# Performance work log

Measured on AMD Instinct MI355X. Metric: run time of the kernel, lower is better.

## Reference

```python
import jax, jax.numpy as jnp
import numpy as np

B, C, H, N, M = 4, 256, 4, 2048, 2048
D = C // H  # head_dim
BN_EPS = 1e-5


def conv1x1(W, b, x):
    # nn.Conv1d(Cin, Cout, kernel_size=1): x [B, Cin, N] -> [B, Cout, N]
    return jnp.einsum('oc,bcn->bon', W, x) + b[None, :, None]


def setup_inputs() -> dict:
    key = jax.random.key(0)
    ks = jax.random.split(key, 10)
    w = lambda k, shape: (jax.random.normal(k, shape, jnp.float32) * 0.05)
    return {
        'x1': jax.random.normal(ks[0], (B, C, N), jnp.float32),
        'x2': jax.random.normal(ks[1], (B, C, M), jnp.float32),
        'kv_mask': jax.random.randint(ks[2], (B, M), 0, 2).astype(bool),
        'Wq': w(ks[3], (C, C)), 'bq': jnp.zeros((C,), jnp.float32),
        'Wk': w(ks[4], (C, C)), 'bk': jnp.zeros((C,), jnp.float32),
        'Wv': w(ks[5], (C, C)), 'bv': jnp.zeros((C,), jnp.float32),
        'Wmh': w(ks[6], (C, C)), 'bmh': jnp.zeros((C,), jnp.float32),
        'W1': w(ks[7], (2 * C, 2 * C)), 'b1': jnp.zeros((2 * C,), jnp.float32),
        'bn_gamma': jnp.ones((2 * C,), jnp.float32),
        'bn_beta': jnp.zeros((2 * C,), jnp.float32),
        'bn_mean': jnp.zeros((2 * C,), jnp.float32),
        'bn_var': jnp.ones((2 * C,), jnp.float32),
        'W2': w(ks[8], (C, 2 * C)), 'b2': jnp.zeros((C,), jnp.float32),
    }


def reference(x1, x2, kv_mask, Wq, bq, Wk, bk, Wv, bv, Wmh, bmh,
              W1, b1, bn_gamma, bn_beta, bn_mean, bn_var, W2, b2):
    bsz = x1.shape[0]
    # 1x1-conv Q/K/V projections, reshaped to [B, H, D, N]
    q = conv1x1(Wq, bq, x1).reshape(bsz, H, D, -1)
    k = conv1x1(Wk, bk, x2).reshape(bsz, H, D, -1)
    v = conv1x1(Wv, bv, x2).reshape(bsz, H, D, -1)

    # full attention: scores [B, H, N, M]
    QK = jnp.einsum('bhdn,bhdm->bhnm', q, k)
    # masked_fill happens BEFORE the 1/sqrt(D) scaling in the original
    QK = jnp.where(kv_mask[:, None, None, :], QK, jnp.float32(-1e6))
    score = jax.nn.softmax(QK / np.float32(np.sqrt(D)), axis=-1)
    add_value = jnp.einsum('bhnm,bhdm->bhdn', score, v).reshape(bsz, H * D, -1)

    add_value = conv1x1(Wmh, bmh, add_value)

    # cat_filter: conv1x1 -> BatchNorm1d (inference stats) -> ReLU -> conv1x1
    cat = jnp.concatenate([x1, add_value], axis=1)  # [B, 2C, N]
    h = conv1x1(W1, b1, cat)
    h = (h - bn_mean[None, :, None]) / jnp.sqrt(bn_var[None, :, None] + BN_EPS)
    h = bn_gamma[None, :, None] * h + bn_beta[None, :, None]
    h = jax.nn.relu(h)
    return x1 + conv1x1(W2, b2, h)
```

## Files before the change

kernel.cpp:

```cpp
#include <hip/hip_runtime.h>
#include <hip/hip_bf16.h>

#define SEQN 2048
#define SEQM 2048
#define CDIM 256
#define NB   4
#define NH   4
#define RDYMAGIC 0x7A3F19C5u

using bf16x8 = __attribute__((ext_vector_type(8))) short;
using f32x4  = __attribute__((ext_vector_type(4))) float;

__device__ inline unsigned short f2bf(float x) {
    __hip_bfloat16 h = __float2bfloat16(x);
    return *reinterpret_cast<unsigned short*>(&h);
}

__global__ __launch_bounds__(256, 4) void qkv_k(
    const float* __restrict__ Wq, const float* __restrict__ Wk,
    const float* __restrict__ Wv,
    const float* __restrict__ x1, const float* __restrict__ x2,
    const float* __restrict__ bq, const float* __restrict__ bk,
    const float* __restrict__ bv,
    unsigned short* __restrict__ qbf, unsigned short* __restrict__ kbf,
    unsigned short* __restrict__ vbf,
    const int* __restrict__ kvm, int* __restrict__ pidx, int* __restrict__ mcnt,
    unsigned int* __restrict__ rdy, float qscale)
{
    __shared__ __align__(16) char qsm[35840];
    const int bid = blockIdx.x, tid = threadIdx.x;

    if (bid < NB) {
        int* sc = reinterpret_cast<int*>(qsm);
        const int b = bid;
        int loc[8], c = 0;
        #pragma unroll
        for (int e = 0; e < 8; ++e) {
            loc[e] = (kvm[(size_t)b * SEQM + tid * 8 + e] != 0) ? 1 : 0;
            c += loc[e];
        }
        sc[tid] = c;
        __syncthreads();
        for (int off = 1; off < 256; off <<= 1) {
            int v = (tid >= off) ? sc[tid - off] : 0;
            __syncthreads();
            sc[tid] += v;
            __syncthreads();
        }
        int p = sc[tid] - c;
        if (tid == 255) mcnt[b] = sc[255];
        #pragma unroll
        for (int e = 0; e < 8; ++e) {
            pidx[(size_t)b * SEQM + tid * 8 + e] = loc[e] ? p : -1;
            p += loc[e];
        }
        __threadfence();
        __syncthreads();
        if (tid == 0)
            __hip_atomic_store(&rdy[b], RDYMAGIC, __ATOMIC_RELEASE,
                               __HIP_MEMORY_SCOPE_AGENT);
        return;
    }

    const int g = bid - NB;
    const int z = g >> 8, t = g & 255;
    const int bx = t & 1, by = t >> 1;

    short (*At)[72] = reinterpret_cast<short(*)[72]>(qsm);
    float (*Ts)[68] = reinterpret_cast<float(*)[68]>(qsm + 18432);

    const float* W = (z == 0) ? Wq : (z == 1) ? Wk : Wv;
    const float* X = (z == 0) ? x1 : x2;
    const float* bias = (z == 0) ? bq : (z == 1) ? bk : bv;

    const int w = tid >> 6, l = tid & 63, lm = l & 15, lg = l >> 4;
    const int o0 = bx * 128, ng0 = by * 64;
    const int b = ng0 >> 11, n0 = ng0 & 2047;
    const int wo = (w >> 1) * 64, wn = (w & 1) * 32;

    f32x4 acc[4][2] = {};
    const int arow = tid >> 2, acol = (tid & 3) * 16;
    const int tr = tid >> 2, tc = (tid & 3) * 16;
    const int tg = (((tc >> 4) ^ ((tr >> 3) & 3)) << 4);

    for (int k0 = 0; k0 < 256; k0 += 64) {
        __syncthreads();
        #pragma unroll
        for (int p = 0; p < 2; ++p) {
            const float* s = &W[(size_t)(o0 + arow + 64 * p) * 256 + k0 + acol];
            unsigned int u[8];
            #pragma unroll
            for (int q = 0; q < 4; ++q) {
                float4 f = *reinterpret_cast<const float4*>(&s[4 * q]);
                u[2 * q]     = (unsigned int)f2bf(f.x) | ((unsigned int)f2bf(f.y) << 16);
                u[2 * q + 1] = (unsigned int)f2bf(f.z) | ((unsigned int)f2bf(f.w) << 16);
            }
            *reinterpret_cast<uint4*>(&At[arow + 64 * p][acol]) =
                make_uint4(u[0], u[1], u[2], u[3]);
            *reinterpret_cast<uint4*>(&At[arow + 64 * p][acol + 8]) =
                make_uint4(u[4], u[5], u[6], u[7]);
        }
        {
            const float* s = &X[((size_t)b * CDIM + k0 + tr) * SEQN + n0 + tc];
            #pragma unroll
            for (int q = 0; q < 4; ++q)
                *reinterpret_cast<float4*>(&Ts[tr][tg + 4 * q]) =
                    *reinterpret_cast<const float4*>(&s[4 * q]);
        }
        __syncthreads();
        #pragma unroll
        for (int kc = 0; kc < 2; ++kc) {
            bf16x8 a[4], bf[2];
            #pragma unroll
            for (int i = 0; i < 4; ++i)
                a[i] = *reinterpret_cast<const bf16x8*>(&At[wo + 16 * i + lm][kc * 32 + lg * 8]);
            #pragma unroll
            for (int j = 0; j < 2; ++j) {
                const int bk0 = kc * 32 + lg * 8;
                const int gcol = (((((wn >> 4) + j)) ^ ((bk0 >> 3) & 3)) << 4) | lm;
                union { unsigned int u[4]; bf16x8 v; } cv;
                #pragma unroll
                for (int e = 0; e < 4; ++e) {
                    float lo = Ts[bk0 + 2 * e][gcol];
                    float hi = Ts[bk0 + 2 * e + 1][gcol];
                    cv.u[e] = (unsigned int)f2bf(lo) | ((unsigned int)f2bf(hi) << 16);
                }
                bf[j] = cv.v;
            }
            #pragma unroll
            for (int i = 0; i < 4; ++i)
                #pragma unroll
                for (int j = 0; j < 2; ++j)
                    acc[i][j] = __builtin_amdgcn_mfma_f32_16x16x32_bf16(a[i], bf[j], acc[i][j], 0, 0, 0);
        }
    }

    if (z != 0) {
        if (tid == 0) {
            while (__hip_atomic_load(&rdy[b], __ATOMIC_ACQUIRE,
                                     __HIP_MEMORY_SCOPE_AGENT) != RDYMAGIC)
                __builtin_amdgcn_s_sleep(2);
        }
        __syncthreads();
    }

    #pragma unroll
    for (int j = 0; j < 2; ++j) {
        const int ng = ng0 + wn + 16 * j + lm;
        const int bb = ng >> 11, n = ng & 2047;
        const int pos = (z == 0) ? n : pidx[(size_t)bb * SEQM + n];
        #pragma unroll
        for (int i = 0; i < 4; ++i) {
            const int ob = o0 + wo + 16 * i + 4 * lg;
            float4 bv4 = *reinterpret_cast<const float4*>(&bias[ob]);
            float v[4] = {acc[i][j][0] + bv4.x, acc[i][j][1] + bv4.y,
                          acc[i][j][2] + bv4.z, acc[i][j][3] + bv4.w};
            if (z == 2) {
                if (pos >= 0) {
                    #pragma unroll
                    for (int r = 0; r < 4; ++r)
                        vbf[((size_t)bb * CDIM + ob + r) * SEQM + pos] = f2bf(v[r]);
                }
            } else if (pos >= 0) {
                const int hh = ob >> 6, dbase = ob & 63;
                const float sc_ = (z == 0) ? qscale : 1.0f;
                ushort4 pk;
                pk.x = f2bf(v[0] * sc_); pk.y = f2bf(v[1] * sc_);
                pk.z = f2bf(v[2] * sc_); pk.w = f2bf(v[3] * sc_);
                unsigned short* dst = (z == 0) ? qbf : kbf;
                *reinterpret_cast<ushort4*>(
                    &dst[(((size_t)bb * NH + hh) * SEQN + pos) * 64 + dbase]) = pk;
            }
        }
    }
}

__device__ void do_attn(char* smraw,
    const unsigned short* __restrict__ qbf, const unsigned short* __restrict__ kbf,
    const unsigned short* __restrict__ vbf, const int* __restrict__ mcntg,
    unsigned short* __restrict__ catT, int bx, int h, int b)
{
    short (*Ks)[64][64] = reinterpret_cast<short(*)[64][64]>(smraw);
    short (*Vs)[64][64] = reinterpret_cast<short(*)[64][64]>(smraw + 16384);
    unsigned int (*Ps)[16][36] = reinterpret_cast<unsigned int(*)[16][36]>(smraw + 32768);

    const int tid = threadIdx.x;
    const int w = tid >> 6, l = tid & 63;
    const int lm = l & 15, lg = l >> 4;
    const int n_base = bx * 64 + w * 16;
    const size_t bhN = (size_t)(b * NH + h) * SEQN;
    const size_t cBase = (size_t)b * CDIM + h * 64;

    const int mcnt = mcntg[b];
    const int ntiles = (mcnt + 63) >> 6;

    if (ntiles == 0) {
        #pragma unroll
        for (int r = 0; r < 4; ++r) {
            int n = n_base + 4 * lg + r;
            unsigned short* dst = &catT[((size_t)b * SEQN + n) * 512 + 256 + h * 64];
            #pragma unroll
            for (int t = 0; t < 4; ++t) dst[16 * t + lm] = 0;
        }
        return;
    }

    const size_t qrow = (bhN + n_base + lm) * 64;
    bf16x8 qa0 = *reinterpret_cast<const bf16x8*>(&qbf[qrow + lg * 8]);
    bf16x8 qa1 = *reinterpret_cast<const bf16x8*>(&qbf[qrow + 32 + lg * 8]);

    f32x4 oacc[4] = {};
    float mrun = -3.0e5f, lrun = 0.f;

    const int r0 = tid >> 3, c8 = (tid & 7) * 8;
    const int c8s = c8 ^ ((r0 & 7) << 3);
    const int colr0 = (lg * 8) ^ ((lm & 7) << 3);
    const int colr1 = (32 + lg * 8) ^ ((lm & 7) << 3);

    {
        bf16x8 kr[2], vr[2];
        #pragma unroll
        for (int p = 0; p < 2; ++p) {
            kr[p] = *reinterpret_cast<const bf16x8*>(&kbf[(bhN + r0 + 32 * p) * 64 + c8]);
            vr[p] = *reinterpret_cast<const bf16x8*>(&vbf[(cBase + r0 + 32 * p) * SEQM + c8]);
        }
        #pragma unroll
        for (int p = 0; p < 2; ++p) {
            *reinterpret_cast<bf16x8*>(&Ks[0][r0 + 32 * p][c8s]) = kr[p];
            *reinterpret_cast<bf16x8*>(&Vs[0][r0 + 32 * p][c8s]) = vr[p];
        }
    }
    __syncthreads();

    for (int t64 = 0; t64 < ntiles; ++t64) {
        const int cur = t64 & 1;
        const bool has_next = (t64 < ntiles - 1);
        const int m0n = (t64 + 1) * 64;

        bf16x8 kr[2], vr[2];
        if (has_next) {
            #pragma unroll
            for (int p = 0; p < 2; ++p) {
                kr[p] = *reinterpret_cast<const bf16x8*>(
                    &kbf[(bhN + m0n + r0 + 32 * p) * 64 + c8]);
                vr[p] = *reinterpret_cast<const bf16x8*>(
                    &vbf[(cBase + r0 + 32 * p) * SEQM + m0n + c8]);
            }
        }

        f32x4 sv[4];
        __builtin_amdgcn_s_setprio(1);
        #pragma unroll
        for (int t = 0; t < 4; ++t) {
            bf16x8 ka0 = *reinterpret_cast<const bf16x8*>(&Ks[cur][16 * t + lm][colr0]);
            bf16x8 ka1 = *reinterpret_cast<const bf16x8*>(&Ks[cur][16 * t + lm][colr1]);
            f32x4 z = {0.f, 0.f, 0.f, 0.f};
            z = __builtin_amdgcn_mfma_f32_16x16x32_bf16(ka0, qa0, z, 0, 0, 0);
            z = __builtin_amdgcn_mfma_f32_16x16x32_bf16(ka1, qa1, z, 0, 0, 0);
            sv[t] = z;
        }
        __builtin_amdgcn_s_setprio(0);

        float mx = fmaxf(fmaxf(fmaxf(sv[0][0], sv[0][1]), fmaxf(sv[0][2], sv[0][3])),
                         fmaxf(fmaxf(sv[1][0], sv[1][1]), fmaxf(sv[1][2], sv[1][3])));
        mx = fmaxf(mx, fmaxf(fmaxf(fmaxf(sv[2][0], sv[2][1]), fmaxf(sv[2][2], sv[2][3])),
                             fmaxf(fmaxf(sv[3][0], sv[3][1]), fmaxf(sv[3][2], sv[3][3]))));
        mx = fmaxf(mx, __shfl_xor(mx, 16));
        mx = fmaxf(mx, __shfl_xor(mx, 32));
        const bool grew = (mx > mrun);
        float mnew = fmaxf(mrun, mx);
        float scl = exp2f(mrun - mnew);
        mrun = mnew;

        float rsum = 0.f;
        const int mrem = mcnt - t64 * 64;
        if (mrem >= 64) {
            #pragma unroll
            for (int t = 0; t < 4; ++t) {
                float p0 = exp2f(sv[t][0] - mnew);
                float p1 = exp2f(sv[t][1] - mnew);
                float p2 = exp2f(sv[t][2] - mnew);
                float p3 = exp2f(sv[t][3] - mnew);
                rsum += (p0 + p1) + (p2 + p3);
                unsigned int u0 = __builtin_amdgcn_perm(
                    __float_as_uint(p1), __float_as_uint(p0), 0x07060302u);
                unsigned int u1 = __builtin_amdgcn_perm(
                    __float_as_uint(p3), __float_as_uint(p2), 0x07060302u);
                *reinterpret_cast<uint2*>(&Ps[w][lm][8 * t + 2 * lg]) = make_uint2(u0, u1);
            }
        } else {
            #pragma unroll
            for (int t = 0; t < 4; ++t) {
                const int mb = 16 * t + 4 * lg;
                float p0 = (mb + 0 < mrem) ? exp2f(sv[t][0] - mnew) : 0.f;
                float p1 = (mb + 1 < mrem) ? exp2f(sv[t][1] - mnew) : 0.f;
                float p2 = (mb + 2 < mrem) ? exp2f(sv[t][2] - mnew) : 0.f;
                float p3 = (mb + 3 < mrem) ? exp2f(sv[t][3] - mnew) : 0.f;
                rsum += (p0 + p1) + (p2 + p3);
                unsigned int u0 = __builtin_amdgcn_perm(
                    __float_as_uint(p1), __float_as_uint(p0), 0x07060302u);
                unsigned int u1 = __builtin_amdgcn_perm(
                    __float_as_uint(p3), __float_as_uint(p2), 0x07060302u);
                *reinterpret_cast<uint2*>(&Ps[w][lm][8 * t + 2 * lg]) = make_uint2(u0, u1);
            }
        }
        rsum += __shfl_xor(rsum, 16);
        rsum += __shfl_xor(rsum, 32);
        lrun = lrun * scl + rsum;

        if (__any(grew && scl < 1.f)) {
            float sr[4];
            #pragma unroll
            for (int r = 0; r < 4; ++r) sr[r] = __shfl(scl, 4 * lg + r);
            #pragma unroll
            for (int t = 0; t < 4; ++t)
                #pragma unroll
                for (int r = 0; r < 4; ++r)
                    oacc[t][r] *= sr[r];
        }

        bf16x8 pa0 = *reinterpret_cast<const bf16x8*>(&Ps[w][lm][4 * lg]);
        bf16x8 pa1 = *reinterpret_cast<const bf16x8*>(&Ps[w][lm][16 + 4 * lg]);
        __builtin_amdgcn_s_setprio(1);
        #pragma unroll
        for (int t = 0; t < 4; ++t) {
            bf16x8 vb0 = *reinterpret_cast<const bf16x8*>(&Vs[cur][16 * t + lm][colr0]);
            bf16x8 vb1 = *reinterpret_cast<const bf16x8*>(&Vs[cur][16 * t + lm][colr1]);
            oacc[t] = __builtin_amdgcn_mfma_f32_16x16x32_bf16(pa0, vb0, oacc[t], 0, 0, 0);
            oacc[t] = __builtin_amdgcn_mfma_f32_16x16x32_bf16(pa1, vb1, oacc[t], 0, 0, 0);
        }
        __builtin_amdgcn_s_setprio(0);

        if (has_next) {
            const int nxt = cur ^ 1;
            #pragma unroll
            for (int p = 0; p < 2; ++p) {
                *reinterpret_cast<bf16x8*>(&Ks[nxt][r0 + 32 * p][c8s]) = kr[p];
                *reinterpret_cast<bf16x8*>(&Vs[nxt][r0 + 32 * p][c8s]) = vr[p];
            }
        }
        __syncthreads();
    }

    #pragma unroll
    for (int r = 0; r < 4; ++r) {
        float rinv = 1.f / __shfl(lrun, 4 * lg + r);
        int n = n_base + 4 * lg + r;
        unsigned short* dst = &catT[((size_t)b * SEQN + n) * 512 + 256 + h * 64];
        #pragma unroll
        for (int t = 0; t < 4; ++t)
            dst[16 * t + lm] = f2bf(oacc[t][r] * rinv);
    }
}

__global__ __launch_bounds__(256) void fused2_k(
    const unsigned short* __restrict__ qbf, const unsigned short* __restrict__ kbf,
    const unsigned short* __restrict__ vbf, const int* __restrict__ mcnt,
    unsigned short* __restrict__ catT,
    const float* __restrict__ W1, const float* __restrict__ b1,
    const float* __restrict__ gamma, const float* __restrict__ beta,
    const float* __restrict__ mean, const float* __restrict__ var,
    const float* __restrict__ Wmh, const float* __restrict__ bmh,
    unsigned short* __restrict__ Acat, float* __restrict__ cvec,
    const float* __restrict__ x1,
    const float* __restrict__ W2, unsigned short* __restrict__ W2b)
{
    __shared__ __align__(16) char smraw[41984];
    const int bid = blockIdx.x, tid = threadIdx.x;

    if (bid < 512) {
        do_attn(smraw, qbf, kbf, vbf, mcnt, catT,
                bid & 31, (bid >> 5) & 3, bid >> 7);
    } else if (bid < 1024) {
        const int j = bid - 512;
        const int c = tid;
        const float s = gamma[j] * rsqrtf(var[j] + 1e-5f);
        const float* w1b = W1 + (size_t)j * 512 + 256;
        Acat[(size_t)j * 512 + c] = f2bf(s * W1[(size_t)j * 512 + c]);
        float acc = 0.f;
        for (int t = 0; t < 256; ++t)
            acc += w1b[t] * Wmh[(size_t)t * 256 + c];
        Acat[(size_t)j * 512 + 256 + c] = f2bf(s * acc);
        if (c == 0) {
            float ab = 0.f;
            for (int t = 0; t < 256; ++t) ab += w1b[t] * bmh[t];
            cvec[j] = s * (b1[j] + ab - mean[j]) + beta[j];
        }
    } else if (bid < 1536) {
        const int t = bid - 1024;
        float (*Ts)[68] = reinterpret_cast<float(*)[68]>(smraw);
        const int cx = t & 3, ny = (t >> 2) & 31, b = t >> 7;
        const int c0 = cx * 64, n0 = ny * 64;
        const int cr = tid >> 2, nc = (tid & 3) * 16;
        #pragma unroll
        for (int q = 0; q < 4; ++q) {
            float4 v = *reinterpret_cast<const float4*>(
                &x1[((size_t)b * CDIM + c0 + cr) * SEQN + n0 + nc + 4 * q]);
            *reinterpret_cast<float4*>(&Ts[cr][nc + 4 * q]) = v;
        }
        __syncthreads();
        const int nr = tid >> 2, cc = (tid & 3) * 16;
        unsigned short tmp[16];
        #pragma unroll
        for (int e = 0; e < 16; ++e) tmp[e] = f2bf(Ts[cc + e][nr]);
        unsigned short* dp = &catT[((size_t)(b * SEQN + n0 + nr)) * 512 + c0 + cc];
        #pragma unroll
        for (int q = 0; q < 4; ++q)
            *reinterpret_cast<ushort4*>(&dp[4 * q]) = *reinterpret_cast<ushort4*>(&tmp[4 * q]);
    } else {
        const int cid = bid - 1536;
        const int idx = (cid * 256 + tid) * 4;
        float4 v = *reinterpret_cast<const float4*>(&W2[idx]);
        ushort4 p; p.x = f2bf(v.x); p.y = f2bf(v.y); p.z = f2bf(v.z); p.w = f2bf(v.w);
        *reinterpret_cast<ushort4*>(&W2b[idx]) = p;
    }
}

template<int OMODE>
__global__ __launch_bounds__(256) void gemm_mfma_k(
    const unsigned short* __restrict__ W, const unsigned short* __restrict__ X,
    const float* __restrict__ bias, const float* __restrict__ res,
    unsigned short* __restrict__ obf, float* __restrict__ ofp,
    int K, int ldx)
{
    __shared__ short At[128][72];
    __shared__ short Bt[64][72];
    const int tid = threadIdx.x;
    const int w = tid >> 6, l = tid & 63, lm = l & 15, lg = l >> 4;
    const int o0 = blockIdx.x * 128, ng0 = blockIdx.y * 64;
    const int wo = (w >> 1) * 64, wn = (w & 1) * 32;

    f32x4 acc[4][2] = {};
    const int arow = tid >> 2, acol = (tid & 3) * 16;

    for (int k0 = 0; k0 < K; k0 += 64) {
        __syncthreads();
        #pragma unroll
        for (int p = 0; p < 2; ++p) {
            const unsigned short* s = &W[(size_t)(o0 + arow + 64 * p) * K + k0 + acol];
            *reinterpret_cast<bf16x8*>(&At[arow + 64 * p][acol]) =
                *reinterpret_cast<const bf16x8*>(s);
            *reinterpret_cast<bf16x8*>(&At[arow + 64 * p][acol + 8]) =
                *reinterpret_cast<const bf16x8*>(s + 8);
        }
        {
            const unsigned short* s = &X[(size_t)(ng0 + arow) * ldx + k0 + acol];
            *reinterpret_cast<bf16x8*>(&Bt[arow][acol]) =
                *reinterpret_cast<const bf16x8*>(s);
            *reinterpret_cast<bf16x8*>(&Bt[arow][acol + 8]) =
                *reinterpret_cast<const bf16x8*>(s + 8);
        }
        __syncthreads();
        #pragma unroll
        for (int kc = 0; kc < 2; ++kc) {
            bf16x8 a[4], bf[2];
            #pragma unroll
            for (int i = 0; i < 4; ++i)
                a[i] = *reinterpret_cast<const bf16x8*>(&At[wo + 16 * i + lm][kc * 32 + lg * 8]);
            #pragma unroll
            for (int j = 0; j < 2; ++j)
                bf[j] = *reinterpret_cast<const bf16x8*>(&Bt[wn + 16 * j + lm][kc * 32 + lg * 8]);
            #pragma unroll
            for (int i = 0; i < 4; ++i)
                #pragma unroll
                for (int j = 0; j < 2; ++j)
                    acc[i][j] = __builtin_amdgcn_mfma_f32_16x16x32_bf16(a[i], bf[j], acc[i][j], 0, 0, 0);
        }
    }

    #pragma unroll
    for (int j = 0; j < 2; ++j) {
        const int ng = ng0 + wn + 16 * j + lm;
        const int b = ng >> 11, n = ng & 2047;
        #pragma unroll
        for (int i = 0; i < 4; ++i) {
            const int ob = o0 + wo + 16 * i + 4 * lg;
            float4 bv = *reinterpret_cast<const float4*>(&bias[ob]);
            float v[4] = {acc[i][j][0] + bv.x, acc[i][j][1] + bv.y,
                          acc[i][j][2] + bv.z, acc[i][j][3] + bv.w};
            if (OMODE == 2) {
                ushort4 pk;
                pk.x = f2bf(fmaxf(v[0], 0.f)); pk.y = f2bf(fmaxf(v[1], 0.f));
                pk.z = f2bf(fmaxf(v[2], 0.f)); pk.w = f2bf(fmaxf(v[3], 0.f));
                *reinterpret_cast<ushort4*>(&obf[(size_t)ng * 512 + ob]) = pk;
            } else {
                #pragma unroll
                for (int r = 0; r < 4; ++r) {
                    size_t ad = ((size_t)b * CDIM + ob + r) * SEQN + n;
                    ofp[ad] = v[r] + res[ad];
                }
            }
        }
    }
}

extern "C" void kernel_launch(void* const* d_in, const int* in_sizes, int n_in,
                              void* d_out, int out_size, void* d_ws, size_t ws_size,
                              hipStream_t stream)
{
    (void)in_sizes; (void)n_in; (void)out_size; (void)ws_size;
    const float* x1    = (const float*)d_in[0];
    const float* x2    = (const float*)d_in[1];
    const int*   kvm   = (const int*)  d_in[2];
    const float* Wq    = (const float*)d_in[3];
    const float* bq    = (const float*)d_in[4];
    const float* Wk    = (const float*)d_in[5];
    const float* bk    = (const float*)d_in[6];
    const float* Wv    = (const float*)d_in[7];
    const float* bv    = (const float*)d_in[8];
    const float* Wmh   = (const float*)d_in[9];
    const float* bmh   = (const float*)d_in[10];
    const float* W1    = (const float*)d_in[11];
    const float* b1    = (const float*)d_in[12];
    const float* gamma = (const float*)d_in[13];
    const float* beta  = (const float*)d_in[14];
    const float* mean  = (const float*)d_in[15];
    const float* var   = (const float*)d_in[16];
    const float* W2    = (const float*)d_in[17];
    const float* b2    = (const float*)d_in[18];
    float* out = (float*)d_out;

    const size_t act = (size_t)NB * CDIM * SEQN;
    unsigned short* ws    = (unsigned short*)d_ws;
    unsigned short* qbf   = ws;
    unsigned short* kbf   = qbf   + act;
    unsigned short* vbf   = kbf   + act;
    unsigned short* catT  = vbf   + act;
    unsigned short* hbuf  = catT  + 2 * act;
    unsigned short* W2b   = hbuf  + 2 * act;
    unsigned short* Acat  = W2b   + 131072;
    float*          cvec  = (float*)(Acat + 262144);
    int*            pidx  = (int*)(cvec + 512);
    int*            mcnt  = pidx + (size_t)NB * SEQM;
    unsigned int*   rdy   = (unsigned int*)(mcnt + 16);

    const float qscale = 0.125f * 1.44269504088896f;

    qkv_k<<<dim3(NB + 768), dim3(256), 0, stream>>>(
        Wq, Wk, Wv, x1, x2, bq, bk, bv, qbf, kbf, vbf,
        kvm, pidx, mcnt, rdy, qscale);

    fused2_k<<<dim3(1664), dim3(256), 0, stream>>>(
        qbf, kbf, vbf, mcnt, catT,
        W1, b1, gamma, beta, mean, var, Wmh, bmh, Acat, cvec,
        x1, W2, W2b);

    gemm_mfma_k<2><<<dim3(4, 128), dim3(256), 0, stream>>>(
        Acat, catT, cvec, nullptr, hbuf, nullptr, 512, 512);

    gemm_mfma_k<3><<<dim3(2, 128), dim3(256), 0, stream>>>(
        W2b, hbuf, b2, x1, nullptr, out, 512, 512);
}
```

Measured before the change: 78.12 us.

## Fuse the two final GEMMs into one launch with per-tile counter handoff

Merges the W1 (BN+ReLU) GEMM and the W2 residual GEMM into a single kernel. Consumer blocks spin on a per-column-tile atomic counter until all four producer row-blocks have written that hbuf tile, which removes one launch and lets the two stages overlap. The block-index mappings in the QKV and attention kernels are also reordered to group tiles per XCD for cache locality. The risks are spin-wait deadlock if consumers occupy CUs before producers run (ordering by block id mitigates this) and the extra counter reset.

```diff
diff --git a/kernel.cpp b/kernel.cpp
--- a/kernel.cpp
+++ b/kernel.cpp
@@ -25,12 +25,14 @@
     unsigned short* __restrict__ qbf, unsigned short* __restrict__ kbf,
     unsigned short* __restrict__ vbf,
     const int* __restrict__ kvm, int* __restrict__ pidx, int* __restrict__ mcnt,
-    unsigned int* __restrict__ rdy, float qscale)
+    unsigned int* __restrict__ rdy, unsigned int* __restrict__ hcnt,
+    float qscale)
 {
     __shared__ __align__(16) char qsm[35840];
     const int bid = blockIdx.x, tid = threadIdx.x;
 
     if (bid < NB) {
+        if (bid == 0 && tid < 128) hcnt[tid] = 0;
         int* sc = reinterpret_cast<int*>(qsm);
         const int b = bid;
         int loc[8], c = 0;
@@ -64,7 +66,7 @@
 
     const int g = bid - NB;
     const int z = g >> 8, t = g & 255;
-    const int bx = t & 1, by = t >> 1;
+    const int bx = t >> 7, by = t & 127;
 
     short (*At)[72] = reinterpret_cast<short(*)[72]>(qsm);
     float (*Ts)[68] = reinterpret_cast<float(*)[68]>(qsm + 18432);
@@ -369,8 +371,10 @@
     const int bid = blockIdx.x, tid = threadIdx.x;
 
     if (bid < 512) {
-        do_attn(smraw, qbf, kbf, vbf, mcnt, catT,
-                bid & 31, (bid >> 5) & 3, bid >> 7);
+        const int xcd = bid & 7, slot = bid >> 3;
+        const int p = xcd * 2 + (slot >> 5);
+        const int qt = slot & 31;
+        do_attn(smraw, qbf, kbf, vbf, mcnt, catT, qt, p & 3, p >> 2);
     } else if (bid < 1024) {
         const int j = bid - 512;
         const int c = tid;
@@ -416,35 +420,54 @@
     }
 }
 
-template<int OMODE>
-__global__ __launch_bounds__(256) void gemm_mfma_k(
-    const unsigned short* __restrict__ W, const unsigned short* __restrict__ X,
-    const float* __restrict__ bias, const float* __restrict__ res,
-    unsigned short* __restrict__ obf, float* __restrict__ ofp,
-    int K, int ldx)
+__global__ __launch_bounds__(256) void gemm23_k(
+    const unsigned short* __restrict__ Acat, const float* __restrict__ cvec,
+    const unsigned short* __restrict__ W2b, const float* __restrict__ b2,
+    const float* __restrict__ x1,
+    const unsigned short* __restrict__ catT, unsigned short* __restrict__ hbuf,
+    float* __restrict__ out, unsigned int* __restrict__ hcnt)
 {
     __shared__ short At[128][72];
     __shared__ short Bt[64][72];
-    const int tid = threadIdx.x;
+    const int bid = blockIdx.x, tid = threadIdx.x;
     const int w = tid >> 6, l = tid & 63, lm = l & 15, lg = l >> 4;
-    const int o0 = blockIdx.x * 128, ng0 = blockIdx.y * 64;
+    const int arow = tid >> 2, acol = (tid & 3) * 16;
     const int wo = (w >> 1) * 64, wn = (w & 1) * 32;
 
+    const bool prod = (bid < 512);
+    const int g = prod ? bid : bid - 512;
+    const int bx = g >> 7, by = g & 127;
+    const int o0 = bx * 128, ng0 = by * 64;
+
+    const unsigned short* W = prod ? Acat : W2b;
+    const unsigned short* X = prod ? catT : hbuf;
+
+    if (!prod) {
+        if (tid == 0) {
+            int sp = 0;
+            while (__hip_atomic_load(&hcnt[by], __ATOMIC_ACQUIRE,
+                                     __HIP_MEMORY_SCOPE_AGENT) < 4u
+                   && sp < 10000000) {
+                __builtin_amdgcn_s_sleep(2);
+                ++sp;
+            }
+        }
+        __syncthreads();
+    }
+
     f32x4 acc[4][2] = {};
-    const int arow = tid >> 2, acol = (tid & 3) * 16;
-
-    for (int k0 = 0; k0 < K; k0 += 64) {
+    for (int k0 = 0; k0 < 512; k0 += 64) {
         __syncthreads();
         #pragma unroll
         for (int p = 0; p < 2; ++p) {
-            const unsigned short* s = &W[(size_t)(o0 + arow + 64 * p) * K + k0 + acol];
+            const unsigned short* s = &W[(size_t)(o0 + arow + 64 * p) * 512 + k0 + acol];
             *reinterpret_cast<bf16x8*>(&At[arow + 64 * p][acol]) =
                 *reinterpret_cast<const bf16x8*>(s);
             *reinterpret_cast<bf16x8*>(&At[arow + 64 * p][acol + 8]) =
                 *reinterpret_cast<const bf16x8*>(s + 8);
         }
         {
-            const unsigned short* s = &X[(size_t)(ng0 + arow) * ldx + k0 + acol];
+            const unsigned short* s = &X[(size_t)(ng0 + arow) * 512 + k0 + acol];
             *reinterpret_cast<bf16x8*>(&Bt[arow][acol]) =
                 *reinterpret_cast<const bf16x8*>(s);
             *reinterpret_cast<bf16x8*>(&Bt[arow][acol + 8]) =
@@ -468,26 +491,42 @@
         }
     }
 
-    #pragma unroll
-    for (int j = 0; j < 2; ++j) {
-        const int ng = ng0 + wn + 16 * j + lm;
-        const int b = ng >> 11, n = ng & 2047;
-        #pragma unroll
-        for (int i = 0; i < 4; ++i) {
-            const int ob = o0 + wo + 16 * i + 4 * lg;
-            float4 bv = *reinterpret_cast<const float4*>(&bias[ob]);
-            float v[4] = {acc[i][j][0] + bv.x, acc[i][j][1] + bv.y,
-                          acc[i][j][2] + bv.z, acc[i][j][3] + bv.w};
-            if (OMODE == 2) {
+    if (prod) {
+        #pragma unroll
+        for (int j = 0; j < 2; ++j) {
+            const int ng = ng0 + wn + 16 * j + lm;
+            #pragma unroll
+            for (int i = 0; i < 4; ++i) {
+                const int ob = o0 + wo + 16 * i + 4 * lg;
+                float4 bv = *reinterpret_cast<const float4*>(&cvec[ob]);
                 ushort4 pk;
-                pk.x = f2bf(fmaxf(v[0], 0.f)); pk.y = f2bf(fmaxf(v[1], 0.f));
-                pk.z = f2bf(fmaxf(v[2], 0.f)); pk.w = f2bf(fmaxf(v[3], 0.f));
-                *reinterpret_cast<ushort4*>(&obf[(size_t)ng * 512 + ob]) = pk;
-            } else {
+                pk.x = f2bf(fmaxf(acc[i][j][0] + bv.x, 0.f));
+                pk.y = f2bf(fmaxf(acc[i][j][1] + bv.y, 0.f));
+                pk.z = f2bf(fmaxf(acc[i][j][2] + bv.z, 0.f));
+                pk.w = f2bf(fmaxf(acc[i][j][3] + bv.w, 0.f));
+                *reinterpret_cast<ushort4*>(&hbuf[(size_t)ng * 512 + ob]) = pk;
+            }
+        }
+        __syncthreads();
+        if (tid == 0) {
+            __threadfence();
+            atomicAdd(&hcnt[by], 1u);
+        }
+    } else {
+        #pragma unroll
+        for (int j = 0; j < 2; ++j) {
+            const int ng = ng0 + wn + 16 * j + lm;
+            const int b = ng >> 11, n = ng & 2047;
+            #pragma unroll
+            for (int i = 0; i < 4; ++i) {
+                const int ob = o0 + wo + 16 * i + 4 * lg;
+                float4 bv = *reinterpret_cast<const float4*>(&b2[ob]);
+                float v[4] = {acc[i][j][0] + bv.x, acc[i][j][1] + bv.y,
+                              acc[i][j][2] + bv.z, acc[i][j][3] + bv.w};
                 #pragma unroll
                 for (int r = 0; r < 4; ++r) {
                     size_t ad = ((size_t)b * CDIM + ob + r) * SEQN + n;
-                    ofp[ad] = v[r] + res[ad];
+                    out[ad] = v[r] + x1[ad];
                 }
             }
         }
@@ -533,21 +572,19 @@
     int*            pidx  = (int*)(cvec + 512);
     int*            mcnt  = pidx + (size_t)NB * SEQM;
     unsigned int*   rdy   = (unsigned int*)(mcnt + 16);
+    unsigned int*   hcnt  = rdy + 16;
 
     const float qscale = 0.125f * 1.44269504088896f;
 
     qkv_k<<<dim3(NB + 768), dim3(256), 0, stream>>>(
         Wq, Wk, Wv, x1, x2, bq, bk, bv, qbf, kbf, vbf,
-        kvm, pidx, mcnt, rdy, qscale);
+        kvm, pidx, mcnt, rdy, hcnt, qscale);
 
     fused2_k<<<dim3(1664), dim3(256), 0, stream>>>(
         qbf, kbf, vbf, mcnt, catT,
         W1, b1, gamma, beta, mean, var, Wmh, bmh, Acat, cvec,
         x1, W2, W2b);
 
-    gemm_mfma_k<2><<<dim3(4, 128), dim3(256), 0, stream>>>(
-        Acat, catT, cvec, nullptr, hbuf, nullptr, 512, 512);
-
-    gemm_mfma_k<3><<<dim3(2, 128), dim3(256), 0, stream>>>(
-        W2b, hbuf, b2, x1, nullptr, out, 512, 512);
+    gemm23_k<<<dim3(768), dim3(256), 0, stream>>>(
+        Acat, cvec, W2b, b2, x1, catT, hbuf, out, hcnt);
 }
```

Result: slower. 120.6 us (+54.4%).

## Move weight folding and x1 transpose into QKV kernel; split attention into own kernel

Applied to the files above, without the earlier changes.

Weight folding (Acat/cvec), the x1 transpose into catT and the W2 bf16 conversion move out of the attention launch and into the QKV projection launch, which gains 1152 extra blocks. Attention becomes a standalone kernel whose block-to-(batch, head, tile) mapping is remapped by XCD so that blocks on the same XCD share K/V for one (b, h). Block index orderings in the QKV and GEMM grids are also changed (1D grid, by-major) to improve L2 locality. The aim is to let attention run with its own smaller LDS footprint and better cache locality, at the cost of a heavier first kernel.

```diff
diff --git a/kernel.cpp b/kernel.cpp
--- a/kernel.cpp
+++ b/kernel.cpp
@@ -25,7 +25,15 @@
     unsigned short* __restrict__ qbf, unsigned short* __restrict__ kbf,
     unsigned short* __restrict__ vbf,
     const int* __restrict__ kvm, int* __restrict__ pidx, int* __restrict__ mcnt,
-    unsigned int* __restrict__ rdy, float qscale)
+    unsigned int* __restrict__ rdy,
+    const float* __restrict__ W1, const float* __restrict__ b1,
+    const float* __restrict__ gamma, const float* __restrict__ beta,
+    const float* __restrict__ mean, const float* __restrict__ var,
+    const float* __restrict__ Wmh, const float* __restrict__ bmh,
+    unsigned short* __restrict__ Acat, float* __restrict__ cvec,
+    unsigned short* __restrict__ catT,
+    const float* __restrict__ W2, unsigned short* __restrict__ W2b,
+    float qscale)
 {
     __shared__ __align__(16) char qsm[35840];
     const int bid = blockIdx.x, tid = threadIdx.x;
@@ -62,9 +70,57 @@
         return;
     }
 
+    if (bid >= NB + 768) {
+        const int xb = bid - (NB + 768);
+        if (xb < 512) {
+            const int j = xb, c = tid;
+            const float s = gamma[j] * rsqrtf(var[j] + 1e-5f);
+            const float* w1b = W1 + (size_t)j * 512 + 256;
+            Acat[(size_t)j * 512 + c] = f2bf(s * W1[(size_t)j * 512 + c]);
+            float acc = 0.f;
+            for (int t = 0; t < 256; ++t)
+                acc += w1b[t] * Wmh[(size_t)t * 256 + c];
+            Acat[(size_t)j * 512 + 256 + c] = f2bf(s * acc);
+            if (c == 0) {
+                float ab = 0.f;
+                for (int t = 0; t < 256; ++t) ab += w1b[t] * bmh[t];
+                cvec[j] = s * (b1[j] + ab - mean[j]) + beta[j];
+            }
+        } else if (xb < 1024) {
+            const int t = xb - 512;
+            float (*Ts)[68] = reinterpret_cast<float(*)[68]>(qsm);
+            const int cx = t & 3, ny = (t >> 2) & 31, b = t >> 7;
+            const int c0 = cx * 64, n0 = ny * 64;
+            const int cr = tid >> 2, nc = (tid & 3) * 16;
+            #pragma unroll
+            for (int q = 0; q < 4; ++q) {
+                float4 v = *reinterpret_cast<const float4*>(
+                    &x1[((size_t)b * CDIM + c0 + cr) * SEQN + n0 + nc + 4 * q]);
+                *reinterpret_cast<float4*>(&Ts[cr][nc + 4 * q]) = v;
+            }
+            __syncthreads();
+            const int nr = tid >> 2, cc = (tid & 3) * 16;
+            unsigned short tmp[16];
+            #pragma unroll
+            for (int e = 0; e < 16; ++e) tmp[e] = f2bf(Ts[cc + e][nr]);
+            unsigned short* dp = &catT[((size_t)(b * SEQN + n0 + nr)) * 512 + c0 + cc];
+            #pragma unroll
+            for (int q = 0; q < 4; ++q)
+                *reinterpret_cast<ushort4*>(&dp[4 * q]) =
+                    *reinterpret_cast<ushort4*>(&tmp[4 * q]);
+        } else {
+            const int cid = xb - 1024;
+            const int idx = (cid * 256 + tid) * 4;
+            float4 v = *reinterpret_cast<const float4*>(&W2[idx]);
+            ushort4 p; p.x = f2bf(v.x); p.y = f2bf(v.y); p.z = f2bf(v.z); p.w = f2bf(v.w);
+            *reinterpret_cast<ushort4*>(&W2b[idx]) = p;
+        }
+        return;
+    }
+
     const int g = bid - NB;
     const int z = g >> 8, t = g & 255;
-    const int bx = t & 1, by = t >> 1;
+    const int bx = t >> 7, by = t & 127;
 
     short (*At)[72] = reinterpret_cast<short(*)[72]>(qsm);
     float (*Ts)[68] = reinterpret_cast<float(*)[68]>(qsm + 18432);
@@ -175,14 +231,19 @@
     }
 }
 
-__device__ void do_attn(char* smraw,
+__global__ __launch_bounds__(256) void attn_mfma_k(
     const unsigned short* __restrict__ qbf, const unsigned short* __restrict__ kbf,
     const unsigned short* __restrict__ vbf, const int* __restrict__ mcntg,
-    unsigned short* __restrict__ catT, int bx, int h, int b)
+    unsigned short* __restrict__ catT)
 {
-    short (*Ks)[64][64] = reinterpret_cast<short(*)[64][64]>(smraw);
-    short (*Vs)[64][64] = reinterpret_cast<short(*)[64][64]>(smraw + 16384);
-    unsigned int (*Ps)[16][36] = reinterpret_cast<unsigned int(*)[16][36]>(smraw + 32768);
+    __shared__ short Ks[2][64][64];
+    __shared__ short Vs[2][64][64];
+    __shared__ unsigned int Ps[4][16][36];
+
+    const int bid = blockIdx.x;
+    const int xcd = bid & 7, slot = bid >> 3;
+    const int p2 = xcd * 2 + (slot >> 5);
+    const int bx = slot & 31, h = p2 & 3, b = p2 >> 2;
 
     const int tid = threadIdx.x;
     const int w = tid >> 6, l = tid & 63;
@@ -353,98 +414,36 @@
     }
 }
 
-__global__ __launch_bounds__(256) void fused2_k(
-    const unsigned short* __restrict__ qbf, const unsigned short* __restrict__ kbf,
-    const unsigned short* __restrict__ vbf, const int* __restrict__ mcnt,
-    unsigned short* __restrict__ catT,
-    const float* __restrict__ W1, const float* __restrict__ b1,
-    const float* __restrict__ gamma, const float* __restrict__ beta,
-    const float* __restrict__ mean, const float* __restrict__ var,
-    const float* __restrict__ Wmh, const float* __restrict__ bmh,
-    unsigned short* __restrict__ Acat, float* __restrict__ cvec,
-    const float* __restrict__ x1,
-    const float* __restrict__ W2, unsigned short* __restrict__ W2b)
-{
-    __shared__ __align__(16) char smraw[41984];
-    const int bid = blockIdx.x, tid = threadIdx.x;
-
-    if (bid < 512) {
-        do_attn(smraw, qbf, kbf, vbf, mcnt, catT,
-                bid & 31, (bid >> 5) & 3, bid >> 7);
-    } else if (bid < 1024) {
-        const int j = bid - 512;
-        const int c = tid;
-        const float s = gamma[j] * rsqrtf(var[j] + 1e-5f);
-        const float* w1b = W1 + (size_t)j * 512 + 256;
-        Acat[(size_t)j * 512 + c] = f2bf(s * W1[(size_t)j * 512 + c]);
-        float acc = 0.f;
-        for (int t = 0; t < 256; ++t)
-            acc += w1b[t] * Wmh[(size_t)t * 256 + c];
-        Acat[(size_t)j * 512 + 256 + c] = f2bf(s * acc);
-        if (c == 0) {
-            float ab = 0.f;
-            for (int t = 0; t < 256; ++t) ab += w1b[t] * bmh[t];
-            cvec[j] = s * (b1[j] + ab - mean[j]) + beta[j];
-        }
-    } else if (bid < 1536) {
-        const int t = bid - 1024;
-        float (*Ts)[68] = reinterpret_cast<float(*)[68]>(smraw);
-        const int cx = t & 3, ny = (t >> 2) & 31, b = t >> 7;
-        const int c0 = cx * 64, n0 = ny * 64;
-        const int cr = tid >> 2, nc = (tid & 3) * 16;
-        #pragma unroll
-        for (int q = 0; q < 4; ++q) {
-            float4 v = *reinterpret_cast<const float4*>(
-                &x1[((size_t)b * CDIM + c0 + cr) * SEQN + n0 + nc + 4 * q]);
-            *reinterpret_cast<float4*>(&Ts[cr][nc + 4 * q]) = v;
-        }
-        __syncthreads();
-        const int nr = tid >> 2, cc = (tid & 3) * 16;
-        unsigned short tmp[16];
-        #pragma unroll
-        for (int e = 0; e < 16; ++e) tmp[e] = f2bf(Ts[cc + e][nr]);
-        unsigned short* dp = &catT[((size_t)(b * SEQN + n0 + nr)) * 512 + c0 + cc];
-        #pragma unroll
-        for (int q = 0; q < 4; ++q)
-            *reinterpret_cast<ushort4*>(&dp[4 * q]) = *reinterpret_cast<ushort4*>(&tmp[4 * q]);
-    } else {
-        const int cid = bid - 1536;
-        const int idx = (cid * 256 + tid) * 4;
-        float4 v = *reinterpret_cast<const float4*>(&W2[idx]);
-        ushort4 p; p.x = f2bf(v.x); p.y = f2bf(v.y); p.z = f2bf(v.z); p.w = f2bf(v.w);
-        *reinterpret_cast<ushort4*>(&W2b[idx]) = p;
-    }
-}
-
 template<int OMODE>
 __global__ __launch_bounds__(256) void gemm_mfma_k(
     const unsigned short* __restrict__ W, const unsigned short* __restrict__ X,
     const float* __restrict__ bias, const float* __restrict__ res,
-    unsigned short* __restrict__ obf, float* __restrict__ ofp,
-    int K, int ldx)
+    unsigned short* __restrict__ obf, float* __restrict__ ofp)
 {
     __shared__ short At[128][72];
     __shared__ short Bt[64][72];
     const int tid = threadIdx.x;
     const int w = tid >> 6, l = tid & 63, lm = l & 15, lg = l >> 4;
-    const int o0 = blockIdx.x * 128, ng0 = blockIdx.y * 64;
+    const int g = blockIdx.x;
+    const int bx = g >> 7, by = g & 127;
+    const int o0 = bx * 128, ng0 = by * 64;
     const int wo = (w >> 1) * 64, wn = (w & 1) * 32;
 
     f32x4 acc[4][2] = {};
     const int arow = tid >> 2, acol = (tid & 3) * 16;
 
-    for (int k0 = 0; k0 < K; k0 += 64) {
+    for (int k0 = 0; k0 < 512; k0 += 64) {
         __syncthreads();
         #pragma unroll
         for (int p = 0; p < 2; ++p) {
-            const unsigned short* s = &W[(size_t)(o0 + arow + 64 * p) * K + k0 + acol];
+            const unsigned short* s = &W[(size_t)(o0 + arow + 64 * p) * 512 + k0 + acol];
             *reinterpret_cast<bf16x8*>(&At[arow + 64 * p][acol]) =
                 *reinterpret_cast<const bf16x8*>(s);
             *reinterpret_cast<bf16x8*>(&At[arow + 64 * p][acol + 8]) =
                 *reinterpret_cast<const bf16x8*>(s + 8);
         }
         {
-            const unsigned short* s = &X[(size_t)(ng0 + arow) * ldx + k0 + acol];
+            const unsigned short* s = &X[(size_t)(ng0 + arow) * 512 + k0 + acol];
             *reinterpret_cast<bf16x8*>(&Bt[arow][acol]) =
                 *reinterpret_cast<const bf16x8*>(s);
             *reinterpret_cast<bf16x8*>(&Bt[arow][acol + 8]) =
@@ -536,18 +535,18 @@
 
     const float qscale = 0.125f * 1.44269504088896f;
 
-    qkv_k<<<dim3(NB + 768), dim3(256), 0, stream>>>(
+    qkv_k<<<dim3(NB + 768 + 1152), dim3(256), 0, stream>>>(
         Wq, Wk, Wv, x1, x2, bq, bk, bv, qbf, kbf, vbf,
-        kvm, pidx, mcnt, rdy, qscale);
-
-    fused2_k<<<dim3(1664), dim3(256), 0, stream>>>(
-        qbf, kbf, vbf, mcnt, catT,
+        kvm, pidx, mcnt, rdy,
         W1, b1, gamma, beta, mean, var, Wmh, bmh, Acat, cvec,
-        x1, W2, W2b);
-
-    gemm_mfma_k<2><<<dim3(4, 128), dim3(256), 0, stream>>>(
-        Acat, catT, cvec, nullptr, hbuf, nullptr, 512, 512);
-
-    gemm_mfma_k<3><<<dim3(2, 128), dim3(256), 0, stream>>>(
-        W2b, hbuf, b2, x1, nullptr, out, 512, 512);
+        catT, W2, W2b, qscale);
+
+    attn_mfma_k<<<dim3(512), dim3(256), 0, stream>>>(
+        qbf, kbf, vbf, mcnt, catT);
+
+    gemm_mfma_k<2><<<dim3(512), dim3(256), 0, stream>>>(
+        Acat, catT, cvec, nullptr, hbuf, nullptr);
+
+    gemm_mfma_k<3><<<dim3(256), dim3(256), 0, stream>>>(
+        W2b, hbuf, b2, x1, nullptr, out);
 }
```

Measured after the change: 91.52 us. 1.17x slower.

## Remap block indices for XCD locality and shrink final GEMM tiles

Applied to the files above, without the earlier changes.

Block-to-tile mappings in the QKV projection and the attention blocks are remapped so that blocks sharing an input column tile (or the same batch/head) land on the same XCD and share its L2. The templated GEMM is split into two specialized kernels with a linear grid and constant K. The last GEMM uses 64x64 tiles, doubling its block count to 512 for better CU occupancy. The cost is more weight reloads per output and fewer MFMAs per LDS load in that kernel.

```diff
diff --git a/kernel.cpp b/kernel.cpp
--- a/kernel.cpp
+++ b/kernel.cpp
@@ -64,7 +64,7 @@
 
     const int g = bid - NB;
     const int z = g >> 8, t = g & 255;
-    const int bx = t & 1, by = t >> 1;
+    const int bx = t >> 7, by = t & 127;
 
     short (*At)[72] = reinterpret_cast<short(*)[72]>(qsm);
     float (*Ts)[68] = reinterpret_cast<float(*)[68]>(qsm + 18432);
@@ -369,8 +369,9 @@
     const int bid = blockIdx.x, tid = threadIdx.x;
 
     if (bid < 512) {
-        do_attn(smraw, qbf, kbf, vbf, mcnt, catT,
-                bid & 31, (bid >> 5) & 3, bid >> 7);
+        const int xcd = bid & 7, slot = bid >> 3;
+        const int p2 = xcd * 2 + (slot >> 5);
+        do_attn(smraw, qbf, kbf, vbf, mcnt, catT, slot & 31, p2 & 3, p2 >> 2);
     } else if (bid < 1024) {
         const int j = bid - 512;
         const int c = tid;
@@ -416,35 +417,34 @@
     }
 }
 
-template<int OMODE>
-__global__ __launch_bounds__(256) void gemm_mfma_k(
+__global__ __launch_bounds__(256) void gemm2_k(
     const unsigned short* __restrict__ W, const unsigned short* __restrict__ X,
-    const float* __restrict__ bias, const float* __restrict__ res,
-    unsigned short* __restrict__ obf, float* __restrict__ ofp,
-    int K, int ldx)
+    const float* __restrict__ bias, unsigned short* __restrict__ obf)
 {
     __shared__ short At[128][72];
     __shared__ short Bt[64][72];
     const int tid = threadIdx.x;
     const int w = tid >> 6, l = tid & 63, lm = l & 15, lg = l >> 4;
-    const int o0 = blockIdx.x * 128, ng0 = blockIdx.y * 64;
+    const int g = blockIdx.x;
+    const int bx = g >> 7, by = g & 127;
+    const int o0 = bx * 128, ng0 = by * 64;
     const int wo = (w >> 1) * 64, wn = (w & 1) * 32;
 
     f32x4 acc[4][2] = {};
     const int arow = tid >> 2, acol = (tid & 3) * 16;
 
-    for (int k0 = 0; k0 < K; k0 += 64) {
+    for (int k0 = 0; k0 < 512; k0 += 64) {
         __syncthreads();
         #pragma unroll
         for (int p = 0; p < 2; ++p) {
-            const unsigned short* s = &W[(size_t)(o0 + arow + 64 * p) * K + k0 + acol];
+            const unsigned short* s = &W[(size_t)(o0 + arow + 64 * p) * 512 + k0 + acol];
             *reinterpret_cast<bf16x8*>(&At[arow + 64 * p][acol]) =
                 *reinterpret_cast<const bf16x8*>(s);
             *reinterpret_cast<bf16x8*>(&At[arow + 64 * p][acol + 8]) =
                 *reinterpret_cast<const bf16x8*>(s + 8);
         }
         {
-            const unsigned short* s = &X[(size_t)(ng0 + arow) * ldx + k0 + acol];
+            const unsigned short* s = &X[(size_t)(ng0 + arow) * 512 + k0 + acol];
             *reinterpret_cast<bf16x8*>(&Bt[arow][acol]) =
                 *reinterpret_cast<const bf16x8*>(s);
             *reinterpret_cast<bf16x8*>(&Bt[arow][acol + 8]) =
@@ -471,24 +471,85 @@
     #pragma unroll
     for (int j = 0; j < 2; ++j) {
         const int ng = ng0 + wn + 16 * j + lm;
+        #pragma unroll
+        for (int i = 0; i < 4; ++i) {
+            const int ob = o0 + wo + 16 * i + 4 * lg;
+            float4 bv = *reinterpret_cast<const float4*>(&bias[ob]);
+            ushort4 pk;
+            pk.x = f2bf(fmaxf(acc[i][j][0] + bv.x, 0.f));
+            pk.y = f2bf(fmaxf(acc[i][j][1] + bv.y, 0.f));
+            pk.z = f2bf(fmaxf(acc[i][j][2] + bv.z, 0.f));
+            pk.w = f2bf(fmaxf(acc[i][j][3] + bv.w, 0.f));
+            *reinterpret_cast<ushort4*>(&obf[(size_t)ng * 512 + ob]) = pk;
+        }
+    }
+}
+
+__global__ __launch_bounds__(256) void gemm3_k(
+    const unsigned short* __restrict__ W, const unsigned short* __restrict__ X,
+    const float* __restrict__ bias, const float* __restrict__ res,
+    float* __restrict__ ofp)
+{
+    __shared__ short At[64][72];
+    __shared__ short Bt[64][72];
+    const int tid = threadIdx.x;
+    const int w = tid >> 6, l = tid & 63, lm = l & 15, lg = l >> 4;
+    const int g = blockIdx.x;
+    const int bx = g >> 7, by = g & 127;
+    const int o0 = bx * 64, ng0 = by * 64;
+    const int wo = (w >> 1) * 32, wn = (w & 1) * 32;
+
+    f32x4 acc[2][2] = {};
+    const int arow = tid >> 2, acol = (tid & 3) * 16;
+
+    for (int k0 = 0; k0 < 512; k0 += 64) {
+        __syncthreads();
+        {
+            const unsigned short* s = &W[(size_t)(o0 + arow) * 512 + k0 + acol];
+            *reinterpret_cast<bf16x8*>(&At[arow][acol]) =
+                *reinterpret_cast<const bf16x8*>(s);
+            *reinterpret_cast<bf16x8*>(&At[arow][acol + 8]) =
+                *reinterpret_cast<const bf16x8*>(s + 8);
+        }
+        {
+            const unsigned short* s = &X[(size_t)(ng0 + arow) * 512 + k0 + acol];
+            *reinterpret_cast<bf16x8*>(&Bt[arow][acol]) =
+                *reinterpret_cast<const bf16x8*>(s);
+            *reinterpret_cast<bf16x8*>(&Bt[arow][acol + 8]) =
+                *reinterpret_cast<const bf16x8*>(s + 8);
+        }
+        __syncthreads();
+        #pragma unroll
+        for (int kc = 0; kc < 2; ++kc) {
+            bf16x8 a[2], bf[2];
+            #pragma unroll
+            for (int i = 0; i < 2; ++i)
+                a[i] = *reinterpret_cast<const bf16x8*>(&At[wo + 16 * i + lm][kc * 32 + lg * 8]);
+            #pragma unroll
+            for (int j = 0; j < 2; ++j)
+                bf[j] = *reinterpret_cast<const bf16x8*>(&Bt[wn + 16 * j + lm][kc * 32 + lg * 8]);
+            #pragma unroll
+            for (int i = 0; i < 2; ++i)
+                #pragma unroll
+                for (int j = 0; j < 2; ++j)
+                    acc[i][j] = __builtin_amdgcn_mfma_f32_16x16x32_bf16(a[i], bf[j], acc[i][j], 0, 0, 0);
+        }
+    }
+
+    #pragma unroll
+    for (int j = 0; j < 2; ++j) {
+        const int ng = ng0 + wn + 16 * j + lm;
         const int b = ng >> 11, n = ng & 2047;
         #pragma unroll
-        for (int i = 0; i < 4; ++i) {
+        for (int i = 0; i < 2; ++i) {
             const int ob = o0 + wo + 16 * i + 4 * lg;
             float4 bv = *reinterpret_cast<const float4*>(&bias[ob]);
             float v[4] = {acc[i][j][0] + bv.x, acc[i][j][1] + bv.y,
                           acc[i][j][2] + bv.z, acc[i][j][3] + bv.w};
-            if (OMODE == 2) {
-                ushort4 pk;
-                pk.x = f2bf(fmaxf(v[0], 0.f)); pk.y = f2bf(fmaxf(v[1], 0.f));
-                pk.z = f2bf(fmaxf(v[2], 0.f)); pk.w = f2bf(fmaxf(v[3], 0.f));
-                *reinterpret_cast<ushort4*>(&obf[(size_t)ng * 512 + ob]) = pk;
-            } else {
-                #pragma unroll
-                for (int r = 0; r < 4; ++r) {
-                    size_t ad = ((size_t)b * CDIM + ob + r) * SEQN + n;
-                    ofp[ad] = v[r] + res[ad];
-                }
+            #pragma unroll
+            for (int r = 0; r < 4; ++r) {
+                size_t ad = ((size_t)b * CDIM + ob + r) * SEQN + n;
+                ofp[ad] = v[r] + res[ad];
             }
         }
     }
@@ -545,9 +606,7 @@
         W1, b1, gamma, beta, mean, var, Wmh, bmh, Acat, cvec,
         x1, W2, W2b);
 
-    gemm_mfma_k<2><<<dim3(4, 128), dim3(256), 0, stream>>>(
-        Acat, catT, cvec, nullptr, hbuf, nullptr, 512, 512);
-
-    gemm_mfma_k<3><<<dim3(2, 128), dim3(256), 0, stream>>>(
-        W2b, hbuf, b2, x1, nullptr, out, 512, 512);
+    gemm2_k<<<dim3(512), dim3(256), 0, stream>>>(Acat, catT, cvec, hbuf);
+
+    gemm3_k<<<dim3(512), dim3(256), 0, stream>>>(W2b, hbuf, b2, x1, out);
 }
```

After: 74.30 us, median of 2. -4.9%, faster.
